# Optimization experiments

Hardware: AMD Instinct MI355X
Metric: run time of the kernel (lower is better)

Reference implementation:

```python
import jax, jax.numpy as jnp
import numpy as np

ENC_DIM, DEC_DIM, ATT_DIM = 2048, 512, 512

def setup_inputs() -> dict:
    key = jax.random.key(0)
    ks = jax.random.split(key, 8)
    s_enc = 1.0 / np.sqrt(ENC_DIM)
    s_dec = 1.0 / np.sqrt(DEC_DIM)
    s_att = 1.0 / np.sqrt(ATT_DIM)
    return {
        "encoder_out": jax.random.normal(ks[0], (256, 196, ENC_DIM), jnp.float32),
        "decoder_hidden": jax.random.normal(ks[1], (256, DEC_DIM), jnp.float32),
        "W_enc": jax.random.uniform(ks[2], (ENC_DIM, ATT_DIM), jnp.float32, -s_enc, s_enc),
        "b_enc": jax.random.uniform(ks[3], (ATT_DIM,), jnp.float32, -s_enc, s_enc),
        "W_dec": jax.random.uniform(ks[4], (DEC_DIM, ATT_DIM), jnp.float32, -s_dec, s_dec),
        "b_dec": jax.random.uniform(ks[5], (ATT_DIM,), jnp.float32, -s_dec, s_dec),
        "W_att": jax.random.uniform(ks[6], (ATT_DIM, 1), jnp.float32, -s_att, s_att),
        "b_att": jax.random.uniform(ks[7], (1,), jnp.float32, -s_att, s_att),
    }

def reference(encoder_out, decoder_hidden, W_enc, b_enc, W_dec, b_dec, W_att, b_att):
    # att1: (B, P, A); att2: (B, 1, A)
    att1 = jnp.einsum('bpe,ea->bpa', encoder_out, W_enc) + b_enc
    att2 = (decoder_hidden @ W_dec + b_dec)[:, None, :]
    # scalar score per pixel: (B, P)
    e = (jax.nn.relu(att1 + att2) @ W_att)[..., 0] + b_att[0]
    alpha = jax.nn.softmax(e, axis=-1)  # softmax over pixels
    z = jnp.einsum('bpe,bp->be', encoder_out, alpha)
    return (z, alpha)
```

## Files before the change

kernel.cpp:

```cpp
#include <hip/hip_runtime.h>
#include <hip/hip_bf16.h>

#define ENC_DIM 2048
#define DEC_DIM 512
#define ATT_DIM 512
#define NB 256
#define NP 196
#define M_TOT (NB * NP)
#define BM 64
#define BK 32
#define NSTEP (ENC_DIM / BK)

typedef __attribute__((ext_vector_type(8))) short short8;
typedef __attribute__((ext_vector_type(4))) short short4s;
typedef __attribute__((ext_vector_type(4))) float f32x4;

__device__ __forceinline__ void gll16(const short* g, short* l) {
    __builtin_amdgcn_global_load_lds((const __attribute__((address_space(1))) void*)g,
                                     (__attribute__((address_space(3))) void*)l,
                                     16, 0, 0);
}

__device__ __forceinline__ short4s cvt4(f32x4 v) {
    union { short4s s; __hip_bfloat16 h[4]; } u;
    u.h[0] = __float2bfloat16(v[0]);
    u.h[1] = __float2bfloat16(v[1]);
    u.h[2] = __float2bfloat16(v[2]);
    u.h[3] = __float2bfloat16(v[3]);
    return u.s;
}

__global__ __launch_bounds__(256) void prep_kernel(const float* __restrict__ W,
                                                   __hip_bfloat16* __restrict__ Btt,
                                                   const float* __restrict__ dec,
                                                   const float* __restrict__ W_dec,
                                                   const float* __restrict__ b_dec,
                                                   const float* __restrict__ b_enc,
                                                   float* __restrict__ att2f) {
    __shared__ float ds[DEC_DIM];
    if (blockIdx.x < 512) {
        const int gid = blockIdx.x * 256 + threadIdx.x;
        const int s   = gid >> 11;
        const int u   = gid & 2047;
        const int cb  = u >> 6;
        const int kg  = (u >> 4) & 3;
        const int l15 = u & 15;
        const int col = cb * 16 + l15;
        const int k0  = s * 32 + kg * 8;
        union { short8 v; __hip_bfloat16 h[8]; } x;
        #pragma unroll
        for (int i = 0; i < 8; ++i)
            x.h[i] = __float2bfloat16(W[(size_t)(k0 + i) * ATT_DIM + col]);
        *(short8*)((short*)Btt + (size_t)gid * 8) = x.v;
    } else {
        const int b = blockIdx.x - 512;
        const int t = threadIdx.x;
        ds[t]       = dec[(size_t)b * DEC_DIM + t];
        ds[t + 256] = dec[(size_t)b * DEC_DIM + t + 256];
        __syncthreads();
        #pragma unroll
        for (int j = 0; j < 2; ++j) {
            const int n = t + j * 256;
            float s = 0.f;
            #pragma unroll 8
            for (int k = 0; k < DEC_DIM; ++k)
                s += ds[k] * W_dec[(size_t)k * ATT_DIM + n];
            att2f[(size_t)b * ATT_DIM + n] = s + b_dec[n] + b_enc[n];
        }
    }
}

__global__ __launch_bounds__(512, 4) void e_kernel(const float* __restrict__ enc,
                                                   const short* __restrict__ Btt,
                                                   const float* __restrict__ att2f,
                                                   const float* __restrict__ W_att,
                                                   float* __restrict__ e_out) {
    __shared__ __attribute__((aligned(16))) short Bs[2][16384];
    __shared__ __attribute__((aligned(16))) short As[2][2048];
    __shared__ float ebuf[8][64];

    const int tid  = threadIdx.x;
    const int lane = tid & 63;
    const int wv   = tid >> 6;
    const int l15  = lane & 15;
    const int kg   = lane >> 4;
    const int M0   = blockIdx.x * BM;

    const int arow = tid >> 3;
    const int aq   = tid & 7;
    const float* asrc = enc + (size_t)(M0 + arow) * ENC_DIM + aq * 4;
    const int awr = (arow >> 4) * 512 + (aq >> 1) * 128 + (arow & 15) * 8 + (aq & 1) * 4;

    const short* bsrc = Btt + (size_t)wv * 512 + lane * 8;

    f32x4 acc[4][4];
    #pragma unroll
    for (int i = 0; i < 4; ++i)
        #pragma unroll
        for (int j = 0; j < 4; ++j)
            acc[i][j] = (f32x4){0.f, 0.f, 0.f, 0.f};

    #pragma unroll
    for (int g = 0; g < 4; ++g)
        gll16(bsrc + g * 4096, &Bs[0][(g * 8 + wv) * 512]);
    {
        f32x4 a0 = *(const f32x4*)asrc;
        *(short4s*)&As[0][awr] = cvt4(a0);
    }
    f32x4 avP, avQ;
    asm volatile("global_load_dwordx4 %0, %1, off" : "=v"(avP)
                 : "v"((unsigned long long)(asrc + 1 * BK)));
    asm volatile("global_load_dwordx4 %0, %1, off" : "=v"(avQ)
                 : "v"((unsigned long long)(asrc + 2 * BK)));
    asm volatile("s_waitcnt lgkmcnt(0)" ::: "memory");

    for (int s = 0; s < NSTEP; ++s) {
        const int cur = s & 1;
        const int nxt = cur ^ 1;
        __builtin_amdgcn_s_barrier();
        asm volatile("s_waitcnt vmcnt(1)" ::: "memory");
        __builtin_amdgcn_sched_barrier(0);

        const int sb = (s + 1) & (NSTEP - 1);
        const short* bs = bsrc + (size_t)sb * 16384;
        #pragma unroll
        for (int g = 0; g < 4; ++g)
            gll16(bs + g * 4096, &Bs[nxt][(g * 8 + wv) * 512]);
        const int sa = (s + 3) & (NSTEP - 1);
        f32x4 avN;
        asm volatile("global_load_dwordx4 %0, %1, off" : "=v"(avN)
                     : "v"((unsigned long long)(asrc + sa * BK)));

        *(short4s*)&As[nxt][awr] = cvt4(avP);
        avP = avQ; avQ = avN;

        short8 af[4];
        #pragma unroll
        for (int mf = 0; mf < 4; ++mf)
            af[mf] = *(const short8*)&As[cur][mf * 512 + lane * 8];
        short8 bf[4];
        #pragma unroll
        for (int nf = 0; nf < 4; ++nf)
            bf[nf] = *(const short8*)&Bs[cur][(wv * 4 + nf) * 512 + lane * 8];

        __builtin_amdgcn_s_setprio(1);
        #pragma unroll
        for (int mf = 0; mf < 4; ++mf)
            #pragma unroll
            for (int nf = 0; nf < 4; ++nf)
                acc[mf][nf] = __builtin_amdgcn_mfma_f32_16x16x32_bf16(af[mf], bf[nf], acc[mf][nf], 0, 0, 0);
        __builtin_amdgcn_s_setprio(0);

        asm volatile("s_waitcnt lgkmcnt(0)" ::: "memory");
        __builtin_amdgcn_sched_barrier(0);
    }

    float wat[4];
    #pragma unroll
    for (int nf = 0; nf < 4; ++nf) wat[nf] = W_att[wv * 64 + nf * 16 + l15];

    #pragma unroll
    for (int mf = 0; mf < 4; ++mf) {
        #pragma unroll
        for (int rr = 0; rr < 4; ++rr) {
            const int ml = mf * 16 + kg * 4 + rr;
            const int bb = (M0 + ml) / NP;
            const float* arow2 = att2f + (size_t)bb * ATT_DIM + wv * 64 + l15;
            float sv = 0.f;
            #pragma unroll
            for (int nf = 0; nf < 4; ++nf) {
                float v = acc[mf][nf][rr] + arow2[nf * 16];
                sv += fmaxf(v, 0.f) * wat[nf];
            }
            sv += __shfl_xor(sv, 1);
            sv += __shfl_xor(sv, 2);
            sv += __shfl_xor(sv, 4);
            sv += __shfl_xor(sv, 8);
            if (l15 == 0) ebuf[wv][ml] = sv;
        }
    }
    __syncthreads();
    if (tid < 64) {
        float sv = 0.f;
        #pragma unroll
        for (int w = 0; w < 8; ++w) sv += ebuf[w][tid];
        e_out[M0 + tid] = sv;
    }
}

__global__ __launch_bounds__(256) void z_kernel(const float* __restrict__ enc,
                                                const float* __restrict__ e,
                                                float* __restrict__ z,
                                                float* __restrict__ alpha) {
    const int b  = blockIdx.x;
    const int cb = blockIdx.y;
    const int t  = threadIdx.x;
    __shared__ float al[NP];
    __shared__ float red[4];

    float ev = (t < NP) ? e[(size_t)b * NP + t] : -1e30f;
    float m = ev;
    #pragma unroll
    for (int o = 32; o > 0; o >>= 1) m = fmaxf(m, __shfl_xor(m, o));
    if ((t & 63) == 0) red[t >> 6] = m;
    __syncthreads();
    m = fmaxf(fmaxf(red[0], red[1]), fmaxf(red[2], red[3]));
    __syncthreads();
    float ex = (t < NP) ? __expf(ev - m) : 0.f;
    float s = ex;
    #pragma unroll
    for (int o = 32; o > 0; o >>= 1) s += __shfl_xor(s, o);
    if ((t & 63) == 0) red[t >> 6] = s;
    __syncthreads();
    s = red[0] + red[1] + red[2] + red[3];
    const float a = ex * (1.0f / s);
    if (t < NP) {
        al[t] = a;
        if (cb == 0) alpha[(size_t)b * NP + t] = a;
    }
    __syncthreads();

    const int c0 = cb * 1024 + t * 4;
    const float4* ep = (const float4*)(enc + (size_t)b * NP * ENC_DIM + c0);
    float4 z0 = make_float4(0.f, 0.f, 0.f, 0.f);
    float4 z1 = make_float4(0.f, 0.f, 0.f, 0.f);
    #pragma unroll 4
    for (int p = 0; p < NP; p += 2) {
        const float a0 = al[p];
        const float a1 = al[p + 1];
        const float4 v0 = ep[(size_t)p * (ENC_DIM / 4)];
        const float4 v1 = ep[(size_t)(p + 1) * (ENC_DIM / 4)];
        z0.x += a0 * v0.x; z0.y += a0 * v0.y; z0.z += a0 * v0.z; z0.w += a0 * v0.w;
        z1.x += a1 * v1.x; z1.y += a1 * v1.y; z1.z += a1 * v1.z; z1.w += a1 * v1.w;
    }
    z0.x += z1.x; z0.y += z1.y; z0.z += z1.z; z0.w += z1.w;
    *(float4*)(z + (size_t)b * ENC_DIM + c0) = z0;
}

extern "C" void kernel_launch(void* const* d_in, const int* in_sizes, int n_in,
                              void* d_out, int out_size, void* d_ws, size_t ws_size,
                              hipStream_t stream) {
    const float* enc   = (const float*)d_in[0];
    const float* dec   = (const float*)d_in[1];
    const float* W_enc = (const float*)d_in[2];
    const float* b_enc = (const float*)d_in[3];
    const float* W_dec = (const float*)d_in[4];
    const float* b_dec = (const float*)d_in[5];
    const float* W_att = (const float*)d_in[6];

    float* z     = (float*)d_out;
    float* alpha = z + (size_t)NB * ENC_DIM;

    char* ws = (char*)d_ws;
    __hip_bfloat16* Btt = (__hip_bfloat16*)ws;
    float* att2f        = (float*)(ws + 2 * 1024 * 1024);
    float* e            = (float*)(ws + 2 * 1024 * 1024 + 512 * 1024);

    prep_kernel<<<768, 256, 0, stream>>>(W_enc, Btt, dec, W_dec, b_dec, b_enc, att2f);
    e_kernel<<<M_TOT / BM, 512, 0, stream>>>(enc, (const short*)Btt, att2f, W_att, e);
    z_kernel<<<dim3(NB, 2), 256, 0, stream>>>(enc, e, z, alpha);
}
```

Before: 313.0 us.

## Load B fragments directly from global into registers, drop LDS staging for weights

Removes the shared-memory double buffer for the pre-packed bf16 weight tile: each wave now loads its own B fragments straight from global (L2-resident) memory into registers one step ahead. The main loop is unrolled by two with explicit register ping-pong, so only the A tile still goes through LDS. This cuts LDS footprint and LDS traffic, which may raise occupancy. In exchange, each block reads its B fragments from global/L2 on every step, and latency hiding now depends on the one-step register prefetch.

```diff
diff --git a/kernel.cpp b/kernel.cpp
--- a/kernel.cpp
+++ b/kernel.cpp
@@ -14,12 +14,6 @@
 typedef __attribute__((ext_vector_type(8))) short short8;
 typedef __attribute__((ext_vector_type(4))) short short4s;
 typedef __attribute__((ext_vector_type(4))) float f32x4;
-
-__device__ __forceinline__ void gll16(const short* g, short* l) {
-    __builtin_amdgcn_global_load_lds((const __attribute__((address_space(1))) void*)g,
-                                     (__attribute__((address_space(3))) void*)l,
-                                     16, 0, 0);
-}
 
 __device__ __forceinline__ short4s cvt4(f32x4 v) {
     union { short4s s; __hip_bfloat16 h[4]; } u;
@@ -42,10 +36,10 @@
         const int gid = blockIdx.x * 256 + threadIdx.x;
         const int s   = gid >> 11;
         const int u   = gid & 2047;
-        const int cb  = u >> 6;
+        const int fr  = u >> 6;
         const int kg  = (u >> 4) & 3;
         const int l15 = u & 15;
-        const int col = cb * 16 + l15;
+        const int col = fr * 16 + l15;
         const int k0  = s * 32 + kg * 8;
         union { short8 v; __hip_bfloat16 h[8]; } x;
         #pragma unroll
@@ -75,7 +69,6 @@
                                                    const float* __restrict__ att2f,
                                                    const float* __restrict__ W_att,
                                                    float* __restrict__ e_out) {
-    __shared__ __attribute__((aligned(16))) short Bs[2][16384];
     __shared__ __attribute__((aligned(16))) short As[2][2048];
     __shared__ float ebuf[8][64];
 
@@ -91,7 +84,7 @@
     const float* asrc = enc + (size_t)(M0 + arow) * ENC_DIM + aq * 4;
     const int awr = (arow >> 4) * 512 + (aq >> 1) * 128 + (arow & 15) * 8 + (aq & 1) * 4;
 
-    const short* bsrc = Btt + (size_t)wv * 512 + lane * 8;
+    const short* pBb = Btt + wv * 2048 + kg * 128 + l15 * 8;
 
     f32x4 acc[4][4];
     #pragma unroll
@@ -100,60 +93,82 @@
         for (int j = 0; j < 4; ++j)
             acc[i][j] = (f32x4){0.f, 0.f, 0.f, 0.f};
 
-    #pragma unroll
-    for (int g = 0; g < 4; ++g)
-        gll16(bsrc + g * 4096, &Bs[0][(g * 8 + wv) * 512]);
-    {
-        f32x4 a0 = *(const f32x4*)asrc;
-        *(short4s*)&As[0][awr] = cvt4(a0);
-    }
-    f32x4 avP, avQ;
-    asm volatile("global_load_dwordx4 %0, %1, off" : "=v"(avP)
-                 : "v"((unsigned long long)(asrc + 1 * BK)));
-    asm volatile("global_load_dwordx4 %0, %1, off" : "=v"(avQ)
-                 : "v"((unsigned long long)(asrc + 2 * BK)));
+#define MFMA16(A0, A1, A2, A3, B0, B1, B2, B3)                                              \
+    acc[0][0] = __builtin_amdgcn_mfma_f32_16x16x32_bf16(A0, B0, acc[0][0], 0, 0, 0);        \
+    acc[0][1] = __builtin_amdgcn_mfma_f32_16x16x32_bf16(A0, B1, acc[0][1], 0, 0, 0);        \
+    acc[0][2] = __builtin_amdgcn_mfma_f32_16x16x32_bf16(A0, B2, acc[0][2], 0, 0, 0);        \
+    acc[0][3] = __builtin_amdgcn_mfma_f32_16x16x32_bf16(A0, B3, acc[0][3], 0, 0, 0);        \
+    acc[1][0] = __builtin_amdgcn_mfma_f32_16x16x32_bf16(A1, B0, acc[1][0], 0, 0, 0);        \
+    acc[1][1] = __builtin_amdgcn_mfma_f32_16x16x32_bf16(A1, B1, acc[1][1], 0, 0, 0);        \
+    acc[1][2] = __builtin_amdgcn_mfma_f32_16x16x32_bf16(A1, B2, acc[1][2], 0, 0, 0);        \
+    acc[1][3] = __builtin_amdgcn_mfma_f32_16x16x32_bf16(A1, B3, acc[1][3], 0, 0, 0);        \
+    acc[2][0] = __builtin_amdgcn_mfma_f32_16x16x32_bf16(A2, B0, acc[2][0], 0, 0, 0);        \
+    acc[2][1] = __builtin_amdgcn_mfma_f32_16x16x32_bf16(A2, B1, acc[2][1], 0, 0, 0);        \
+    acc[2][2] = __builtin_amdgcn_mfma_f32_16x16x32_bf16(A2, B2, acc[2][2], 0, 0, 0);        \
+    acc[2][3] = __builtin_amdgcn_mfma_f32_16x16x32_bf16(A2, B3, acc[2][3], 0, 0, 0);        \
+    acc[3][0] = __builtin_amdgcn_mfma_f32_16x16x32_bf16(A3, B0, acc[3][0], 0, 0, 0);        \
+    acc[3][1] = __builtin_amdgcn_mfma_f32_16x16x32_bf16(A3, B1, acc[3][1], 0, 0, 0);        \
+    acc[3][2] = __builtin_amdgcn_mfma_f32_16x16x32_bf16(A3, B2, acc[3][2], 0, 0, 0);        \
+    acc[3][3] = __builtin_amdgcn_mfma_f32_16x16x32_bf16(A3, B3, acc[3][3], 0, 0, 0);
+
+    *(short4s*)&As[0][awr] = cvt4(*(const f32x4*)asrc);
+    short8 c0 = *(const short8*)(pBb);
+    short8 c1 = *(const short8*)(pBb + 512);
+    short8 c2 = *(const short8*)(pBb + 1024);
+    short8 c3 = *(const short8*)(pBb + 1536);
+    f32x4 avP = *(const f32x4*)(asrc + BK);
     asm volatile("s_waitcnt lgkmcnt(0)" ::: "memory");
-
-    for (int s = 0; s < NSTEP; ++s) {
-        const int cur = s & 1;
-        const int nxt = cur ^ 1;
+    __builtin_amdgcn_s_barrier();
+    __builtin_amdgcn_sched_barrier(0);
+
+    for (int s = 0; s < NSTEP; s += 2) {
+        const short* p1 = pBb + (size_t)((s + 1) & 63) * 16384;
+        short8 n0 = *(const short8*)(p1);
+        short8 n1 = *(const short8*)(p1 + 512);
+        short8 n2 = *(const short8*)(p1 + 1024);
+        short8 n3 = *(const short8*)(p1 + 1536);
+        f32x4 avN0 = *(const f32x4*)(asrc + (size_t)((s + 2) & 63) * BK);
+        __builtin_amdgcn_sched_barrier(0);
+        {
+            const short* Ac = &As[0][0];
+            const short8 a0 = *(const short8*)&Ac[0 * 512 + lane * 8];
+            const short8 a1 = *(const short8*)&Ac[1 * 512 + lane * 8];
+            const short8 a2 = *(const short8*)&Ac[2 * 512 + lane * 8];
+            const short8 a3 = *(const short8*)&Ac[3 * 512 + lane * 8];
+            __builtin_amdgcn_s_setprio(1);
+            MFMA16(a0, a1, a2, a3, c0, c1, c2, c3)
+            __builtin_amdgcn_s_setprio(0);
+        }
+        *(short4s*)&As[1][awr] = cvt4(avP);
+        avP = avN0;
+        asm volatile("s_waitcnt lgkmcnt(0)" ::: "memory");
         __builtin_amdgcn_s_barrier();
-        asm volatile("s_waitcnt vmcnt(1)" ::: "memory");
-        __builtin_amdgcn_sched_barrier(0);
-
-        const int sb = (s + 1) & (NSTEP - 1);
-        const short* bs = bsrc + (size_t)sb * 16384;
-        #pragma unroll
-        for (int g = 0; g < 4; ++g)
-            gll16(bs + g * 4096, &Bs[nxt][(g * 8 + wv) * 512]);
-        const int sa = (s + 3) & (NSTEP - 1);
-        f32x4 avN;
-        asm volatile("global_load_dwordx4 %0, %1, off" : "=v"(avN)
-                     : "v"((unsigned long long)(asrc + sa * BK)));
-
-        *(short4s*)&As[nxt][awr] = cvt4(avP);
-        avP = avQ; avQ = avN;
-
-        short8 af[4];
-        #pragma unroll
-        for (int mf = 0; mf < 4; ++mf)
-            af[mf] = *(const short8*)&As[cur][mf * 512 + lane * 8];
-        short8 bf[4];
-        #pragma unroll
-        for (int nf = 0; nf < 4; ++nf)
-            bf[nf] = *(const short8*)&Bs[cur][(wv * 4 + nf) * 512 + lane * 8];
-
-        __builtin_amdgcn_s_setprio(1);
-        #pragma unroll
-        for (int mf = 0; mf < 4; ++mf)
-            #pragma unroll
-            for (int nf = 0; nf < 4; ++nf)
-                acc[mf][nf] = __builtin_amdgcn_mfma_f32_16x16x32_bf16(af[mf], bf[nf], acc[mf][nf], 0, 0, 0);
-        __builtin_amdgcn_s_setprio(0);
-
+        __builtin_amdgcn_sched_barrier(0);
+
+        const short* p2 = pBb + (size_t)((s + 2) & 63) * 16384;
+        c0 = *(const short8*)(p2);
+        c1 = *(const short8*)(p2 + 512);
+        c2 = *(const short8*)(p2 + 1024);
+        c3 = *(const short8*)(p2 + 1536);
+        f32x4 avN1 = *(const f32x4*)(asrc + (size_t)((s + 3) & 63) * BK);
+        __builtin_amdgcn_sched_barrier(0);
+        {
+            const short* Ac = &As[1][0];
+            const short8 a0 = *(const short8*)&Ac[0 * 512 + lane * 8];
+            const short8 a1 = *(const short8*)&Ac[1 * 512 + lane * 8];
+            const short8 a2 = *(const short8*)&Ac[2 * 512 + lane * 8];
+            const short8 a3 = *(const short8*)&Ac[3 * 512 + lane * 8];
+            __builtin_amdgcn_s_setprio(1);
+            MFMA16(a0, a1, a2, a3, n0, n1, n2, n3)
+            __builtin_amdgcn_s_setprio(0);
+        }
+        *(short4s*)&As[0][awr] = cvt4(avP);
+        avP = avN1;
         asm volatile("s_waitcnt lgkmcnt(0)" ::: "memory");
-        __builtin_amdgcn_sched_barrier(0);
-    }
+        __builtin_amdgcn_s_barrier();
+        __builtin_amdgcn_sched_barrier(0);
+    }
+#undef MFMA16
 
     float wat[4];
     #pragma unroll
```

After: 321.1 us. 2.6% more time.
